# Kernel optimization log

Hardware: AMD Instinct MI355X
Metric: run time of the kernel (lower is better)

The kernel has to match this reference:

```python
import jax, jax.numpy as jnp
import numpy as np

NEG_SLOPE = 0.2

def gat_conv(x, edge_index, W, a_src, a_dst, bias, heads, channels):
    # PyG GATConv (add_self_loops=False, dropout off in eval)
    N = x.shape[0]
    h = (x @ W).reshape(N, heads, channels)               # [N,H,C]
    src, dst = edge_index[0], edge_index[1]
    e_src = jnp.einsum('nhc,hc->nh', h, a_src)            # [N,H]
    e_dst = jnp.einsum('nhc,hc->nh', h, a_dst)
    e = jax.nn.leaky_relu(e_src[src] + e_dst[dst], NEG_SLOPE)  # [E,H]
    # softmax over incoming edges of each destination node
    m = jax.ops.segment_max(e, dst, num_segments=N)       # [N,H]
    ex = jnp.exp(e - m[dst])
    s = jax.ops.segment_sum(ex, dst, num_segments=N)
    alpha = ex / (s[dst] + 1e-16)                         # [E,H]
    msg = h[src] * alpha[:, :, None]                      # [E,H,C]
    out = jax.ops.segment_sum(msg, dst, num_segments=N)   # [N,H,C]
    return out.reshape(N, heads * channels) + bias


def setup_inputs() -> dict:
    key = jax.random.key(0)
    ks = jax.random.split(key, 12)
    N, E, SED, HID, H, F_OUT = 20000, 320000, 768, 128, 4, 128
    return {
        'x': jax.random.normal(ks[0], (N, SED), jnp.float32),
        'edge_index': jax.random.randint(ks[1], (2, E), 0, N, jnp.int32),
        'sentence_embedding': jax.random.normal(ks[2], (SED,), jnp.float32),
        'W1': jax.random.normal(ks[3], (2 * SED, H * HID), jnp.float32) * 0.02,
        'a1_src': jax.random.normal(ks[4], (H, HID), jnp.float32) * 0.1,
        'a1_dst': jax.random.normal(ks[5], (H, HID), jnp.float32) * 0.1,
        'b1': jax.random.normal(ks[6], (H * HID,), jnp.float32) * 0.02,
        'W2': jax.random.normal(ks[7], (H * HID, F_OUT), jnp.float32) * 0.02,
        'a2_src': jax.random.normal(ks[8], (1, F_OUT), jnp.float32) * 0.1,
        'a2_dst': jax.random.normal(ks[9], (1, F_OUT), jnp.float32) * 0.1,
        'b2': jax.random.normal(ks[10], (F_OUT,), jnp.float32) * 0.02,
    }


def reference(x, edge_index, sentence_embedding, W1, a1_src, a1_dst, b1, W2, a2_src, a2_dst, b2):
    N = x.shape[0]
    sent = jnp.broadcast_to(sentence_embedding[None, :], (N, sentence_embedding.shape[0]))
    h = jnp.concatenate([x, sent], axis=1)                # [N, 2*SED]
    h = gat_conv(h, edge_index, W1, a1_src, a1_dst, b1, heads=4, channels=128)
    h = jax.nn.elu(h)
    out = gat_conv(h, edge_index, W2, a2_src, a2_dst, b2, heads=1, channels=128)
    return out
```

## Files before the change

kernel.cpp:

```cpp
#include <hip/hip_runtime.h>
#include <cstdint>
#include <cstddef>

#define NSLOPE 0.2f

typedef __attribute__((ext_vector_type(8))) short bf16x8;
typedef __attribute__((ext_vector_type(4))) float f32x4;
typedef __attribute__((ext_vector_type(2))) float f32x2;
typedef unsigned short ushort_t;

__device__ inline ushort_t f2bf(float f) {
    union { float f; unsigned u; } v; v.f = f;
    unsigned u = v.u;
    unsigned r = (u + 0x7fffu + ((u >> 16) & 1u)) >> 16;
    return (ushort_t)r;
}
__device__ inline float bf2f(ushort_t u) {
    union { unsigned u; float f; } v; v.u = ((unsigned)u) << 16;
    return v.f;
}
__device__ inline f32x2 unpack2(unsigned u) {
    union { unsigned u; float f; } lo, hi;
    lo.u = u << 16;
    hi.u = u & 0xffff0000u;
    f32x2 r; r.x = lo.f; r.y = hi.f;
    return r;
}
__device__ inline float leaky(float v) { return (v > 0.f) ? v : NSLOPE * v; }
__device__ inline float sel4(float4 q, bool b1, bool b2) {
    return b2 ? (b1 ? q.w : q.z) : (b1 ? q.y : q.x);
}

__global__ __launch_bounds__(256) void prep_kernel(
    const float* __restrict__ x, ushort_t* __restrict__ x_bf16, size_t nx,
    const float* __restrict__ W1, ushort_t* __restrict__ W1T,
    const float* __restrict__ W2, ushort_t* __restrict__ W2T,
    const float* __restrict__ sent, float* __restrict__ svec_part,
    int* __restrict__ indeg, int N, int nbCast, int nbZero)
{
    __shared__ float tile[32][33];
    int bid = blockIdx.x;
    int tid = threadIdx.x;
    if (bid < nbCast) {
        size_t i = ((size_t)bid * 256 + tid) * 8;
        if (i < nx) {
            float4 v0 = *(const float4*)(x + i);
            float4 v1 = *(const float4*)(x + i + 4);
            ushort_t r[8] = { f2bf(v0.x), f2bf(v0.y), f2bf(v0.z), f2bf(v0.w),
                              f2bf(v1.x), f2bf(v1.y), f2bf(v1.z), f2bf(v1.w) };
            *(uint4*)(x_bf16 + i) = *(uint4*)r;
        }
        return;
    }
    bid -= nbCast;
    if (bid < 384) {
        int k0 = (bid % 24) * 32, n0 = (bid / 24) * 32;
        int tx = tid & 31, ty = tid >> 5;
#pragma unroll
        for (int i = 0; i < 4; ++i)
            tile[ty + i * 8][tx] = W1[(size_t)(k0 + ty + i * 8) * 512 + n0 + tx];
        __syncthreads();
#pragma unroll
        for (int i = 0; i < 4; ++i)
            W1T[(size_t)(n0 + ty + i * 8) * 768 + k0 + tx] = f2bf(tile[tx][ty + i * 8]);
        return;
    }
    bid -= 384;
    if (bid < 64) {
        int k0 = (bid % 16) * 32, n0 = (bid / 16) * 32;
        int tx = tid & 31, ty = tid >> 5;
#pragma unroll
        for (int i = 0; i < 4; ++i)
            tile[ty + i * 8][tx] = W2[(size_t)(k0 + ty + i * 8) * 128 + n0 + tx];
        __syncthreads();
#pragma unroll
        for (int i = 0; i < 4; ++i)
            W2T[(size_t)(n0 + ty + i * 8) * 512 + k0 + tx] = f2bf(tile[tx][ty + i * 8]);
        return;
    }
    bid -= 64;
    if (bid < 16) {
        int cb = bid & 1, kb = bid >> 1;
        int c = cb * 256 + tid;
        int k0 = kb * 96;
        float acc = 0.f;
#pragma unroll 8
        for (int k = k0; k < k0 + 96; ++k)
            acc += sent[k] * W1[(size_t)(768 + k) * 512 + c];
        svec_part[kb * 512 + c] = acc;
        return;
    }
    bid -= 16;
    {
        int i = bid * 256 + tid;
        if (i < N) indeg[i] = 0;
    }
}

__device__ inline void async_copy16(const void* g, void* l) {
    __builtin_amdgcn_global_load_lds(
        (const __attribute__((address_space(1))) unsigned int*)g,
        (__attribute__((address_space(3))) unsigned int*)l, 16, 0, 0);
}

__global__ __launch_bounds__(256) void mfma_gemm_kernel(
    const ushort_t* __restrict__ A,
    const ushort_t* __restrict__ BT,
    const float* __restrict__ bias,
    ushort_t* __restrict__ Cb,
    const float* __restrict__ asrc,
    const float* __restrict__ adst,
    float* __restrict__ e_src,
    float* __restrict__ e_dst,
    int eStride,
    int M, int K, int Nc)
{
    __shared__ __align__(16) ushort_t lA[3][128 * 32];
    __shared__ __align__(16) ushort_t lB[3][128 * 32];
    __shared__ float e_lds[128][2][2];
    const int tid = threadIdx.x;
    const int wave = tid >> 6;
    const int lane = tid & 63;

    const int h = blockIdx.y * gridDim.x + blockIdx.x;
    const int xcd = h & 7;
    const int slot = h >> 3;
    const int by = xcd + 8 * (slot / gridDim.x);
    const int bx = slot % gridDim.x;

    const int col0 = bx * 128;
    const int row0 = by * 128;
    const int wm = (wave & 1) * 64;
    const int wn = (wave >> 1) * 64;
    const int q = lane >> 4;
    const int ml = lane & 15;

    f32x4 acc[4][4] = {};

    int rowS[2], gS[2];
#pragma unroll
    for (int i = 0; i < 2; ++i) {
        int p = wave * 128 + i * 64 + lane;
        int r = p >> 2, s = p & 3;
        rowS[i] = r;
        gS[i] = s ^ ((r >> 1) & 3);
    }

    auto stage = [&](int k0, int buf) {
#pragma unroll
        for (int i = 0; i < 2; ++i) {
            int pb = wave * 128 + i * 64;
            int r = rowS[i];
            int ga = min(row0 + r, M - 1);
            async_copy16(A + (size_t)ga * K + k0 + gS[i] * 8, &lA[buf][(size_t)pb * 8]);
            async_copy16(BT + (size_t)(col0 + r) * K + k0 + gS[i] * 8, &lB[buf][(size_t)pb * 8]);
        }
    };

    const int nt = K >> 5;
    stage(0, 0);
    if (nt > 1) {
        stage(32, 1);
        asm volatile("s_waitcnt vmcnt(4)\n\ts_barrier" ::: "memory");
    } else {
        asm volatile("s_waitcnt vmcnt(0)\n\ts_barrier" ::: "memory");
    }

    for (int t = 0; t < nt; ++t) {
        const int pb = t % 3;
        if (t + 2 < nt) stage((t + 2) << 5, (t + 2) % 3);
        bf16x8 af[4], bfr[4];
#pragma unroll
        for (int tt = 0; tt < 4; ++tt) {
            int m = wm + tt * 16 + ml;
            af[tt] = *(const bf16x8*)&lA[pb][(size_t)(m * 4 + (q ^ ((m >> 1) & 3))) * 8];
            int n = wn + tt * 16 + ml;
            bfr[tt] = *(const bf16x8*)&lB[pb][(size_t)(n * 4 + (q ^ ((n >> 1) & 3))) * 8];
        }
#pragma unroll
        for (int tm = 0; tm < 4; ++tm)
#pragma unroll
            for (int tn = 0; tn < 4; ++tn)
                acc[tm][tn] = __builtin_amdgcn_mfma_f32_16x16x32_bf16(
                    af[tm], bfr[tn], acc[tm][tn], 0, 0, 0);
        if (t + 2 < nt)
            asm volatile("s_waitcnt vmcnt(4) lgkmcnt(0)\n\ts_barrier" ::: "memory");
        else if (t + 1 < nt)
            asm volatile("s_waitcnt vmcnt(0) lgkmcnt(0)\n\ts_barrier" ::: "memory");
    }

    float es_acc[4][4] = {};
    float ed_acc[4][4] = {};
#pragma unroll
    for (int tm = 0; tm < 4; ++tm) {
        int rbase = row0 + wm + tm * 16 + q * 4;
#pragma unroll
        for (int tn = 0; tn < 4; ++tn) {
            int col = col0 + wn + tn * 16 + ml;
            float bb = bias ? bias[col] : 0.f;
            float av = asrc[col];
            float dv = adst[col];
#pragma unroll
            for (int r = 0; r < 4; ++r) {
                int row = rbase + r;
                float val = acc[tm][tn][r] + bb;
                if (row < M)
                    Cb[(size_t)row * Nc + col] = f2bf(val);
                es_acc[tm][r] += val * av;
                ed_acc[tm][r] += val * dv;
            }
        }
    }
    const int colhalf = wave >> 1;
#pragma unroll
    for (int tm = 0; tm < 4; ++tm) {
#pragma unroll
        for (int r = 0; r < 4; ++r) {
            float es = es_acc[tm][r], ed2 = ed_acc[tm][r];
#pragma unroll
            for (int st = 1; st < 16; st <<= 1) {
                es += __shfl_xor(es, st);
                ed2 += __shfl_xor(ed2, st);
            }
            if (ml == 0) {
                int rl = wm + tm * 16 + q * 4 + r;
                e_lds[rl][colhalf][0] = es;
                e_lds[rl][colhalf][1] = ed2;
            }
        }
    }
    __syncthreads();
    if (tid < 128) {
        int row = row0 + tid;
        if (row < M) {
            float es = e_lds[tid][0][0] + e_lds[tid][1][0];
            float ed2 = e_lds[tid][0][1] + e_lds[tid][1][1];
            e_src[(size_t)row * eStride + bx] = es;
            e_dst[(size_t)row * eStride + bx] = ed2;
        }
    }
}

__global__ void count_kernel(const int* __restrict__ ei, int* __restrict__ indeg, int E) {
    int e = blockIdx.x * blockDim.x + threadIdx.x;
    if (e < E) atomicAdd(&indeg[ei[E + e]], 1);
}

__global__ __launch_bounds__(1024) void scan_kernel(const int* __restrict__ indeg,
                                                    int* __restrict__ offsets,
                                                    int* __restrict__ cursor,
                                                    const float* __restrict__ svec_part,
                                                    float* __restrict__ svec, int N) {
    __shared__ int partial[1024];
    int tid = threadIdx.x;
    if (tid < 512) {
        float s = 0.f;
#pragma unroll
        for (int kb = 0; kb < 8; ++kb) s += svec_part[kb * 512 + tid];
        svec[tid] = s;
    }
    int per = (N + 1023) / 1024;
    int start = tid * per;
    int end = min(start + per, N);
    int sum = 0;
    if (start + per <= N && (per & 3) == 0) {
        for (int i = 0; i < per; i += 4) {
            int4 v = *(const int4*)(indeg + start + i);
            sum += v.x + v.y + v.z + v.w;
        }
    } else {
        for (int i = start; i < end; ++i) sum += indeg[i];
    }
    partial[tid] = sum;
    __syncthreads();
    for (int st = 1; st < 1024; st <<= 1) {
        int v = (tid >= st) ? partial[tid - st] : 0;
        __syncthreads();
        partial[tid] += v;
        __syncthreads();
    }
    int run = (tid == 0) ? 0 : partial[tid - 1];
    if (start + per <= N && (per & 3) == 0) {
        for (int i = 0; i < per; i += 4) {
            int4 v = *(const int4*)(indeg + start + i);
            int4 o;
            o.x = run;
            o.y = o.x + v.x;
            o.z = o.y + v.y;
            o.w = o.z + v.z;
            run = o.w + v.w;
            *(int4*)(offsets + start + i) = o;
            *(int4*)(cursor + start + i) = o;
        }
    } else {
        for (int i = start; i < end; ++i) {
            offsets[i] = run; cursor[i] = run;
            run += indeg[i];
        }
    }
    if (tid == 1023) offsets[N] = run;
}

__global__ void scatter_kernel(const int* __restrict__ ei, int* __restrict__ cursor,
                               int* __restrict__ csr_src, int E) {
    int e = blockIdx.x * blockDim.x + threadIdx.x;
    if (e < E) {
        int d = ei[E + e];
        int p = atomicAdd(&cursor[d], 1);
        csr_src[p] = ei[e];
    }
}

__global__ __launch_bounds__(256) void gather1_kernel(
    const ushort_t* __restrict__ h1b, const float* __restrict__ e_src,
    const float* __restrict__ e_dst, const int* __restrict__ offsets,
    const int* __restrict__ csr_src, const float* __restrict__ bias,
    ushort_t* __restrict__ outb, int N)
{
    int node = __builtin_amdgcn_readfirstlane(blockIdx.x * 4 + (threadIdx.x >> 6));
    int lane = threadIdx.x & 63;
    if (node >= N) return;
    int beg = offsets[node], end = offsets[node + 1];
    float4 ed = *(const float4*)&e_dst[node * 4];

    const int h = lane >> 4;
    const bool b1 = (h & 1), b2 = (h & 2);
    float edh = sel4(ed, b1, b2);

    const ushort_t* hp = h1b + lane * 8;
    f32x2 acc[4] = {};
    float s = 0.f;
    int j = beg;
#pragma unroll 2
    for (; j + 4 <= end; j += 4) {
        int s0 = csr_src[j], s1 = csr_src[j + 1];
        int s2 = csr_src[j + 2], s3 = csr_src[j + 3];
        float4 q0 = *(const float4*)&e_src[s0 * 4];
        float4 q1 = *(const float4*)&e_src[s1 * 4];
        float4 q2 = *(const float4*)&e_src[s2 * 4];
        float4 q3 = *(const float4*)&e_src[s3 * 4];
        float w0 = __expf(leaky(sel4(q0, b1, b2) + edh));
        float w1 = __expf(leaky(sel4(q1, b1, b2) + edh));
        float w2 = __expf(leaky(sel4(q2, b1, b2) + edh));
        float w3 = __expf(leaky(sel4(q3, b1, b2) + edh));
        s += (w0 + w1) + (w2 + w3);
        uint4 u0 = *(const uint4*)&hp[(size_t)s0 * 512];
        uint4 u1 = *(const uint4*)&hp[(size_t)s1 * 512];
        uint4 u2 = *(const uint4*)&hp[(size_t)s2 * 512];
        uint4 u3 = *(const uint4*)&hp[(size_t)s3 * 512];
        f32x2 wv;
        wv.x = w0; wv.y = w0;
        acc[0] += unpack2(u0.x) * wv; acc[1] += unpack2(u0.y) * wv;
        acc[2] += unpack2(u0.z) * wv; acc[3] += unpack2(u0.w) * wv;
        wv.x = w1; wv.y = w1;
        acc[0] += unpack2(u1.x) * wv; acc[1] += unpack2(u1.y) * wv;
        acc[2] += unpack2(u1.z) * wv; acc[3] += unpack2(u1.w) * wv;
        wv.x = w2; wv.y = w2;
        acc[0] += unpack2(u2.x) * wv; acc[1] += unpack2(u2.y) * wv;
        acc[2] += unpack2(u2.z) * wv; acc[3] += unpack2(u2.w) * wv;
        wv.x = w3; wv.y = w3;
        acc[0] += unpack2(u3.x) * wv; acc[1] += unpack2(u3.y) * wv;
        acc[2] += unpack2(u3.z) * wv; acc[3] += unpack2(u3.w) * wv;
    }
    for (; j < end; ++j) {
        int s0 = csr_src[j];
        float4 q0 = *(const float4*)&e_src[s0 * 4];
        float w0 = __expf(leaky(sel4(q0, b1, b2) + edh));
        s += w0;
        uint4 u0 = *(const uint4*)&hp[(size_t)s0 * 512];
        f32x2 wv; wv.x = w0; wv.y = w0;
        acc[0] += unpack2(u0.x) * wv; acc[1] += unpack2(u0.y) * wv;
        acc[2] += unpack2(u0.z) * wv; acc[3] += unpack2(u0.w) * wv;
    }
    float rs = 1.f / (s + 1e-16f);
    int c = lane * 8;
    ushort_t o[8];
#pragma unroll
    for (int i = 0; i < 4; ++i) {
        float r0 = acc[i].x * rs + bias[c + 2 * i];
        float r1 = acc[i].y * rs + bias[c + 2 * i + 1];
        r0 = (r0 > 0.f) ? r0 : (__expf(r0) - 1.f);
        r1 = (r1 > 0.f) ? r1 : (__expf(r1) - 1.f);
        o[2 * i] = f2bf(r0);
        o[2 * i + 1] = f2bf(r1);
    }
    *(uint4*)&outb[(size_t)node * 512 + c] = *(uint4*)o;
}

__global__ __launch_bounds__(256) void gather2_kernel(
    const ushort_t* __restrict__ h2b, const float* __restrict__ e_src,
    const float* __restrict__ e_dst, const int* __restrict__ offsets,
    const int* __restrict__ csr_src, const float* __restrict__ bias,
    float* __restrict__ out, int N)
{
    int node = __builtin_amdgcn_readfirstlane(blockIdx.x * 4 + (threadIdx.x >> 6));
    int lane = threadIdx.x & 63;
    if (node >= N) return;
    int beg = offsets[node], end = offsets[node + 1];
    float ed = e_dst[node];

    const ushort_t* hp = h2b + lane * 2;
    f32x2 acc = { 0.f, 0.f };
    float s = 0.f;
    int j = beg;
#pragma unroll 2
    for (; j + 4 <= end; j += 4) {
        int s0 = csr_src[j], s1 = csr_src[j + 1];
        int s2 = csr_src[j + 2], s3 = csr_src[j + 3];
        float w0 = __expf(leaky(e_src[s0] + ed));
        float w1 = __expf(leaky(e_src[s1] + ed));
        float w2 = __expf(leaky(e_src[s2] + ed));
        float w3 = __expf(leaky(e_src[s3] + ed));
        s += (w0 + w1) + (w2 + w3);
        unsigned u0 = *(const unsigned*)&hp[(size_t)s0 * 128];
        unsigned u1 = *(const unsigned*)&hp[(size_t)s1 * 128];
        unsigned u2 = *(const unsigned*)&hp[(size_t)s2 * 128];
        unsigned u3 = *(const unsigned*)&hp[(size_t)s3 * 128];
        f32x2 w0v = { w0, w0 }, w1v = { w1, w1 }, w2v = { w2, w2 }, w3v = { w3, w3 };
        acc += unpack2(u0) * w0v;
        acc += unpack2(u1) * w1v;
        acc += unpack2(u2) * w2v;
        acc += unpack2(u3) * w3v;
    }
    for (; j < end; ++j) {
        int s0 = csr_src[j];
        float w0 = __expf(leaky(e_src[s0] + ed));
        s += w0;
        unsigned u0 = *(const unsigned*)&hp[(size_t)s0 * 128];
        f32x2 w0v = { w0, w0 };
        acc += unpack2(u0) * w0v;
    }
    float rs = 1.f / (s + 1e-16f);
    float2 o = make_float2(acc.x * rs + bias[lane * 2], acc.y * rs + bias[lane * 2 + 1]);
    *(float2*)&out[(size_t)node * 128 + lane * 2] = o;
}

extern "C" void kernel_launch(void* const* d_in, const int* in_sizes, int n_in,
                              void* d_out, int out_size, void* d_ws, size_t ws_size,
                              hipStream_t stream) {
    const float* x      = (const float*)d_in[0];
    const int*   ei     = (const int*)  d_in[1];
    const float* sent   = (const float*)d_in[2];
    const float* W1     = (const float*)d_in[3];
    const float* a1_src = (const float*)d_in[4];
    const float* a1_dst = (const float*)d_in[5];
    const float* b1     = (const float*)d_in[6];
    const float* W2     = (const float*)d_in[7];
    const float* a2_src = (const float*)d_in[8];
    const float* a2_dst = (const float*)d_in[9];
    const float* b2     = (const float*)d_in[10];
    float* out = (float*)d_out;

    const int N = in_sizes[0] / 768;
    const int E = in_sizes[1] / 2;

    char* p = (char*)d_ws;
    auto carve = [&](size_t bytes) {
        char* q = p;
        p += (bytes + 255) & ~(size_t)255;
        return q;
    };
    ushort_t* h1b = (ushort_t*)carve((size_t)N * 512 * 2);
    char* shared_region = carve((size_t)N * 768 * 2);
    ushort_t* x_bf16 = (ushort_t*)shared_region;
    ushort_t* h_elu_b = (ushort_t*)shared_region;
    ushort_t* h2b = (ushort_t*)carve((size_t)N * 128 * 2);
    ushort_t* W1T = (ushort_t*)carve((size_t)512 * 768 * 2);
    ushort_t* W2T = (ushort_t*)carve((size_t)128 * 512 * 2);
    float* svec_part = (float*)carve(8 * 512 * 4);
    float* svec   = (float*)carve(512 * 4);
    float* e_src1 = (float*)carve((size_t)N * 4 * 4);
    float* e_dst1 = (float*)carve((size_t)N * 4 * 4);
    float* e_src2 = (float*)carve((size_t)N * 4);
    float* e_dst2 = (float*)carve((size_t)N * 4);
    int*   indeg  = (int*)carve((size_t)N * 4);
    int*   offs   = (int*)carve((size_t)(N + 1) * 4);
    int*   cursor = (int*)carve((size_t)N * 4);
    int*   csrsrc = (int*)carve((size_t)E * 4);

    size_t nx = (size_t)N * 768;
    int nbCast = (int)((nx / 8 + 255) / 256);
    int nbZero = (N + 255) / 256;
    int nbPrep = nbCast + 384 + 64 + 16 + nbZero;

    prep_kernel<<<nbPrep, 256, 0, stream>>>(x, x_bf16, nx, W1, W1T, W2, W2T,
                                            sent, svec_part, indeg, N, nbCast, nbZero);
    count_kernel<<<(E + 255) / 256, 256, 0, stream>>>(ei, indeg, E);
    scan_kernel<<<1, 1024, 0, stream>>>(indeg, offs, cursor, svec_part, svec, N);
    scatter_kernel<<<(E + 255) / 256, 256, 0, stream>>>(ei, cursor, csrsrc, E);

    int nyPad = (((N + 127) / 128) + 7) & ~7;

    mfma_gemm_kernel<<<dim3(4, nyPad), 256, 0, stream>>>(
        x_bf16, W1T, svec, h1b, a1_src, a1_dst, e_src1, e_dst1, 4, N, 768, 512);

    gather1_kernel<<<(N + 3) / 4, 256, 0, stream>>>(
        h1b, e_src1, e_dst1, offs, csrsrc, b1, h_elu_b, N);

    mfma_gemm_kernel<<<dim3(1, nyPad), 256, 0, stream>>>(
        h_elu_b, W2T, nullptr, h2b, a2_src, a2_dst, e_src2, e_dst2, 1, N, 512, 128);

    gather2_kernel<<<(N + 3) / 4, 256, 0, stream>>>(
        h2b, e_src2, e_dst2, offs, csrsrc, b2, out, N);
}
```

Before: 290.1 us.

## Fuse fp32-to-bf16 cast of x into first GEMM's A-tile loading

Removes the separate cast pass over x in the prep kernel; the first GEMM now loads fp32 x tiles into registers, converts them to bf16 and writes them to LDS, while B still uses async LDS copies. This eliminates a full write and re-read of a bf16 copy of x. In exchange, the GEMM reads twice as many bytes for A per column block, and register pressure and wait scheduling increase. The h_elu buffer gets its own allocation since the shared region is gone.

New measurement: 304.3 us. 4.9% more time.

```diff
diff --git a/kernel.cpp b/kernel.cpp
--- a/kernel.cpp
+++ b/kernel.cpp
@@ -14,10 +14,6 @@
     unsigned u = v.u;
     unsigned r = (u + 0x7fffu + ((u >> 16) & 1u)) >> 16;
     return (ushort_t)r;
-}
-__device__ inline float bf2f(ushort_t u) {
-    union { unsigned u; float f; } v; v.u = ((unsigned)u) << 16;
-    return v.f;
 }
 __device__ inline f32x2 unpack2(unsigned u) {
     union { unsigned u; float f; } lo, hi;
@@ -32,27 +28,14 @@
 }
 
 __global__ __launch_bounds__(256) void prep_kernel(
-    const float* __restrict__ x, ushort_t* __restrict__ x_bf16, size_t nx,
     const float* __restrict__ W1, ushort_t* __restrict__ W1T,
     const float* __restrict__ W2, ushort_t* __restrict__ W2T,
     const float* __restrict__ sent, float* __restrict__ svec_part,
-    int* __restrict__ indeg, int N, int nbCast, int nbZero)
+    int* __restrict__ indeg, int N, int nbZero)
 {
     __shared__ float tile[32][33];
     int bid = blockIdx.x;
     int tid = threadIdx.x;
-    if (bid < nbCast) {
-        size_t i = ((size_t)bid * 256 + tid) * 8;
-        if (i < nx) {
-            float4 v0 = *(const float4*)(x + i);
-            float4 v1 = *(const float4*)(x + i + 4);
-            ushort_t r[8] = { f2bf(v0.x), f2bf(v0.y), f2bf(v0.z), f2bf(v0.w),
-                              f2bf(v1.x), f2bf(v1.y), f2bf(v1.z), f2bf(v1.w) };
-            *(uint4*)(x_bf16 + i) = *(uint4*)r;
-        }
-        return;
-    }
-    bid -= nbCast;
     if (bid < 384) {
         int k0 = (bid % 24) * 32, n0 = (bid / 24) * 32;
         int tx = tid & 31, ty = tid >> 5;
@@ -103,8 +86,9 @@
         (__attribute__((address_space(3))) unsigned int*)l, 16, 0, 0);
 }
 
+template <bool AFP32>
 __global__ __launch_bounds__(256) void mfma_gemm_kernel(
-    const ushort_t* __restrict__ A,
+    const void* __restrict__ Ain,
     const ushort_t* __restrict__ BT,
     const float* __restrict__ bias,
     ushort_t* __restrict__ Cb,
@@ -122,9 +106,9 @@
     const int wave = tid >> 6;
     const int lane = tid & 63;
 
-    const int h = blockIdx.y * gridDim.x + blockIdx.x;
-    const int xcd = h & 7;
-    const int slot = h >> 3;
+    const int hh = blockIdx.y * gridDim.x + blockIdx.x;
+    const int xcd = hh & 7;
+    const int slot = hh >> 3;
     const int by = xcd + 8 * (slot / gridDim.x);
     const int bx = slot % gridDim.x;
 
@@ -135,6 +119,9 @@
     const int q = lane >> 4;
     const int ml = lane & 15;
 
+    const float* A32 = (const float*)Ain;
+    const ushort_t* A16 = (const ushort_t*)Ain;
+
     f32x4 acc[4][4] = {};
 
     int rowS[2], gS[2];
@@ -146,47 +133,127 @@
         gS[i] = s ^ ((r >> 1) & 3);
     }
 
-    auto stage = [&](int k0, int buf) {
-#pragma unroll
-        for (int i = 0; i < 2; ++i) {
-            int pb = wave * 128 + i * 64;
-            int r = rowS[i];
-            int ga = min(row0 + r, M - 1);
-            async_copy16(A + (size_t)ga * K + k0 + gS[i] * 8, &lA[buf][(size_t)pb * 8]);
-            async_copy16(BT + (size_t)(col0 + r) * K + k0 + gS[i] * 8, &lB[buf][(size_t)pb * 8]);
-        }
-    };
-
     const int nt = K >> 5;
-    stage(0, 0);
-    if (nt > 1) {
-        stage(32, 1);
-        asm volatile("s_waitcnt vmcnt(4)\n\ts_barrier" ::: "memory");
+
+    if constexpr (!AFP32) {
+        auto stage = [&](int k0, int buf) {
+#pragma unroll
+            for (int i = 0; i < 2; ++i) {
+                int pbs = wave * 128 + i * 64;
+                int r = rowS[i];
+                int ga = min(row0 + r, M - 1);
+                async_copy16(A16 + (size_t)ga * K + k0 + gS[i] * 8, &lA[buf][(size_t)pbs * 8]);
+                async_copy16(BT + (size_t)(col0 + r) * K + k0 + gS[i] * 8, &lB[buf][(size_t)pbs * 8]);
+            }
+        };
+        stage(0, 0);
+        if (nt > 1) {
+            stage(32, 1);
+            asm volatile("s_waitcnt vmcnt(4)\n\ts_barrier" ::: "memory");
+        } else {
+            asm volatile("s_waitcnt vmcnt(0)\n\ts_barrier" ::: "memory");
+        }
+        for (int t = 0; t < nt; ++t) {
+            const int pb = t % 3;
+            if (t + 2 < nt) stage((t + 2) << 5, (t + 2) % 3);
+            bf16x8 af[4], bfr[4];
+#pragma unroll
+            for (int tt = 0; tt < 4; ++tt) {
+                int m = wm + tt * 16 + ml;
+                af[tt] = *(const bf16x8*)&lA[pb][(size_t)(m * 4 + (q ^ ((m >> 1) & 3))) * 8];
+                int n = wn + tt * 16 + ml;
+                bfr[tt] = *(const bf16x8*)&lB[pb][(size_t)(n * 4 + (q ^ ((n >> 1) & 3))) * 8];
+            }
+#pragma unroll
+            for (int tm = 0; tm < 4; ++tm)
+#pragma unroll
+                for (int tn = 0; tn < 4; ++tn)
+                    acc[tm][tn] = __builtin_amdgcn_mfma_f32_16x16x32_bf16(
+                        af[tm], bfr[tn], acc[tm][tn], 0, 0, 0);
+            if (t + 2 < nt)
+                asm volatile("s_waitcnt vmcnt(4) lgkmcnt(0)\n\ts_barrier" ::: "memory");
+            else if (t + 1 < nt)
+                asm volatile("s_waitcnt vmcnt(0) lgkmcnt(0)\n\ts_barrier" ::: "memory");
+        }
     } else {
-        asm volatile("s_waitcnt vmcnt(0)\n\ts_barrier" ::: "memory");
-    }
-
-    for (int t = 0; t < nt; ++t) {
-        const int pb = t % 3;
-        if (t + 2 < nt) stage((t + 2) << 5, (t + 2) % 3);
-        bf16x8 af[4], bfr[4];
-#pragma unroll
-        for (int tt = 0; tt < 4; ++tt) {
-            int m = wm + tt * 16 + ml;
-            af[tt] = *(const bf16x8*)&lA[pb][(size_t)(m * 4 + (q ^ ((m >> 1) & 3))) * 8];
-            int n = wn + tt * 16 + ml;
-            bfr[tt] = *(const bf16x8*)&lB[pb][(size_t)(n * 4 + (q ^ ((n >> 1) & 3))) * 8];
-        }
-#pragma unroll
-        for (int tm = 0; tm < 4; ++tm)
-#pragma unroll
-            for (int tn = 0; tn < 4; ++tn)
-                acc[tm][tn] = __builtin_amdgcn_mfma_f32_16x16x32_bf16(
-                    af[tm], bfr[tn], acc[tm][tn], 0, 0, 0);
-        if (t + 2 < nt)
-            asm volatile("s_waitcnt vmcnt(4) lgkmcnt(0)\n\ts_barrier" ::: "memory");
-        else if (t + 1 < nt)
+        auto loadA = [&](int k0, float4 (&dst)[4]) {
+#pragma unroll
+            for (int i = 0; i < 2; ++i) {
+                int ga = min(row0 + rowS[i], M - 1);
+                const float* src = A32 + (size_t)ga * K + k0 + gS[i] * 8;
+                dst[2 * i]     = *(const float4*)src;
+                dst[2 * i + 1] = *(const float4*)(src + 4);
+            }
+        };
+        auto stageB = [&](int k0, int buf) {
+#pragma unroll
+            for (int i = 0; i < 2; ++i) {
+                int pbs = wave * 128 + i * 64;
+                async_copy16(BT + (size_t)(col0 + rowS[i]) * K + k0 + gS[i] * 8,
+                             &lB[buf][(size_t)pbs * 8]);
+            }
+        };
+        auto cvtWrite = [&](int buf, float4 (&cur)[4]) {
+#pragma unroll
+            for (int i = 0; i < 2; ++i) {
+                float4 lo = cur[2 * i], hi = cur[2 * i + 1];
+                ushort_t tmp[8] = { f2bf(lo.x), f2bf(lo.y), f2bf(lo.z), f2bf(lo.w),
+                                    f2bf(hi.x), f2bf(hi.y), f2bf(hi.z), f2bf(hi.w) };
+                *(uint4*)&lA[buf][(size_t)(wave * 128 + i * 64 + lane) * 8] = *(uint4*)tmp;
+            }
+        };
+
+        float4 rEven[4], rOdd[4];
+        loadA(0, rOdd);
+        stageB(0, 0);
+        if (nt > 1) {
+            loadA(32, rEven);
+            stageB(32, 1);
+            asm volatile("s_waitcnt vmcnt(8)" ::: "memory");
+            cvtWrite(0, rOdd);
+            asm volatile("s_waitcnt vmcnt(6) lgkmcnt(0)\n\ts_barrier" ::: "memory");
+        } else {
+            asm volatile("s_waitcnt vmcnt(2)" ::: "memory");
+            cvtWrite(0, rOdd);
             asm volatile("s_waitcnt vmcnt(0) lgkmcnt(0)\n\ts_barrier" ::: "memory");
+        }
+
+        auto body = [&](int t, float4 (&cur)[4], float4 (&nxt)[4]) {
+            const int pb = t % 3;
+            const bool has2 = (t + 2 < nt);
+            if (has2) {
+                int k0n = (t + 2) << 5;
+                loadA(k0n, nxt);
+                stageB(k0n, (t + 2) % 3);
+            }
+            bf16x8 af[4], bfr[4];
+#pragma unroll
+            for (int tt = 0; tt < 4; ++tt) {
+                int m = wm + tt * 16 + ml;
+                af[tt] = *(const bf16x8*)&lA[pb][(size_t)(m * 4 + (q ^ ((m >> 1) & 3))) * 8];
+                int n = wn + tt * 16 + ml;
+                bfr[tt] = *(const bf16x8*)&lB[pb][(size_t)(n * 4 + (q ^ ((n >> 1) & 3))) * 8];
+            }
+#pragma unroll
+            for (int tm = 0; tm < 4; ++tm)
+#pragma unroll
+                for (int tn = 0; tn < 4; ++tn)
+                    acc[tm][tn] = __builtin_amdgcn_mfma_f32_16x16x32_bf16(
+                        af[tm], bfr[tn], acc[tm][tn], 0, 0, 0);
+            if (t + 1 < nt) {
+                if (has2) asm volatile("s_waitcnt vmcnt(8)" ::: "memory");
+                else      asm volatile("s_waitcnt vmcnt(2)" ::: "memory");
+                cvtWrite((t + 1) % 3, cur);
+                if (has2) asm volatile("s_waitcnt vmcnt(6) lgkmcnt(0)\n\ts_barrier" ::: "memory");
+                else      asm volatile("s_waitcnt vmcnt(0) lgkmcnt(0)\n\ts_barrier" ::: "memory");
+            }
+        };
+
+        for (int t = 0; t + 1 < nt; t += 2) {
+            body(t, rEven, rOdd);
+            body(t + 1, rOdd, rEven);
+        }
+        if (nt & 1) body(nt - 1, rEven, rOdd);
     }
 
     float es_acc[4][4] = {};
@@ -461,9 +528,7 @@
         return q;
     };
     ushort_t* h1b = (ushort_t*)carve((size_t)N * 512 * 2);
-    char* shared_region = carve((size_t)N * 768 * 2);
-    ushort_t* x_bf16 = (ushort_t*)shared_region;
-    ushort_t* h_elu_b = (ushort_t*)shared_region;
+    ushort_t* h_elu_b = (ushort_t*)carve((size_t)N * 512 * 2);
     ushort_t* h2b = (ushort_t*)carve((size_t)N * 128 * 2);
     ushort_t* W1T = (ushort_t*)carve((size_t)512 * 768 * 2);
     ushort_t* W2T = (ushort_t*)carve((size_t)128 * 512 * 2);
@@ -478,26 +543,24 @@
     int*   cursor = (int*)carve((size_t)N * 4);
     int*   csrsrc = (int*)carve((size_t)E * 4);
 
-    size_t nx = (size_t)N * 768;
-    int nbCast = (int)((nx / 8 + 255) / 256);
     int nbZero = (N + 255) / 256;
-    int nbPrep = nbCast + 384 + 64 + 16 + nbZero;
-
-    prep_kernel<<<nbPrep, 256, 0, stream>>>(x, x_bf16, nx, W1, W1T, W2, W2T,
-                                            sent, svec_part, indeg, N, nbCast, nbZero);
+    int nbPrep = 384 + 64 + 16 + nbZero;
+
+    prep_kernel<<<nbPrep, 256, 0, stream>>>(W1, W1T, W2, W2T,
+                                            sent, svec_part, indeg, N, nbZero);
     count_kernel<<<(E + 255) / 256, 256, 0, stream>>>(ei, indeg, E);
     scan_kernel<<<1, 1024, 0, stream>>>(indeg, offs, cursor, svec_part, svec, N);
     scatter_kernel<<<(E + 255) / 256, 256, 0, stream>>>(ei, cursor, csrsrc, E);
 
     int nyPad = (((N + 127) / 128) + 7) & ~7;
 
-    mfma_gemm_kernel<<<dim3(4, nyPad), 256, 0, stream>>>(
-        x_bf16, W1T, svec, h1b, a1_src, a1_dst, e_src1, e_dst1, 4, N, 768, 512);
+    mfma_gemm_kernel<true><<<dim3(4, nyPad), 256, 0, stream>>>(
+        x, W1T, svec, h1b, a1_src, a1_dst, e_src1, e_dst1, 4, N, 768, 512);
 
     gather1_kernel<<<(N + 3) / 4, 256, 0, stream>>>(
         h1b, e_src1, e_dst1, offs, csrsrc, b1, h_elu_b, N);
 
-    mfma_gemm_kernel<<<dim3(1, nyPad), 256, 0, stream>>>(
+    mfma_gemm_kernel<false><<<dim3(1, nyPad), 256, 0, stream>>>(
         h_elu_b, W2T, nullptr, h2b, a2_src, a2_dst, e_src2, e_dst2, 1, N, 512, 128);
 
     gather2_kernel<<<(N + 3) / 4, 256, 0, stream>>>(
```
